# Performance work log

Measured on AMD Instinct MI355X. Metric: run time of the kernel, lower is better.

The kernel has to match this reference:

```python
import jax, jax.numpy as jnp
import numpy as np

EPS = 1e-5
D_MODEL = 64
D_STATE = 16
D_INNER = 128  # expand=2
DT_RANK = 4    # ceil(64/16)


def _inorm(x):
    # InstanceNorm2d (affine=False), NCHW, biased variance, eps=1e-5
    mu = jnp.mean(x, axis=(2, 3), keepdims=True)
    var = jnp.var(x, axis=(2, 3), keepdims=True)
    return (x - mu) * jax.lax.rsqrt(var + EPS)


def _conv2d(x, w, b=None, groups=1):
    y = jax.lax.conv_general_dilated(x, w, (1, 1), 'SAME',
        dimension_numbers=('NCHW', 'OIHW', 'NCHW'), feature_group_count=groups)
    return y if b is None else y + b[None, :, None, None]


def _layernorm(x, w, b):
    mu = jnp.mean(x, axis=-1, keepdims=True)
    var = jnp.var(x, axis=-1, keepdims=True)
    return (x - mu) * jax.lax.rsqrt(var + EPS) * w + b


def _selective_scan(u, delta, A, Bm, Cm, Dp, delta_bias):
    # u, delta: (B,d,L); A: (d,N); Bm,Cm: (B,N,L); Dp: (d,)
    delta = jax.nn.softplus(delta + delta_bias[None, :, None])
    dA = jnp.exp(jnp.einsum('bdl,dn->lbdn', delta, A))        # (L,B,d,N)
    dBu = jnp.einsum('bdl,bnl->lbdn', delta * u, Bm)          # (L,B,d,N)
    Cl = jnp.transpose(Cm, (2, 0, 1))                         # (L,B,N)
    h0 = jnp.zeros((u.shape[0], u.shape[1], A.shape[1]), u.dtype)

    def step(h, inp):
        dA_l, dBu_l, c = inp
        h = dA_l * h + dBu_l
        return h, jnp.einsum('bdn,bn->bd', h, c)

    _, ys = jax.lax.scan(step, h0, (dA, dBu, Cl))             # ys: (L,B,d)
    return jnp.transpose(ys, (1, 2, 0)) + u * Dp[None, :, None]


def _forward(x, dw3_w, dw3_b, dw5_w, dw5_b, dw7_w, dw7_b, fuse_w, fuse_b,
             in_proj_w, conv2d_w, conv2d_b, x_proj_w, dt_proj_w, dt_proj_b,
             A_log, Dp, out_norm_w, out_norm_b, out_proj_w, cf_w, cf_b):
    C = x.shape[1]
    lrelu = lambda t: jax.nn.leaky_relu(t, 0.01)
    # ---- LRGS: multi-scale depthwise convs + fuse + residual (shortcut=Identity) ----
    feats = [lrelu(_inorm(_conv2d(x, w, b, groups=C)))
             for w, b in ((dw3_w, dw3_b), (dw5_w, dw5_b), (dw7_w, dw7_b))]
    xf = _conv2d(jnp.concatenate(feats, axis=1), fuse_w, fuse_b)
    x1 = lrelu(_inorm(xf)) + x
    # ---- MC_Mamba / SS2D ----
    xh = jnp.transpose(x1, (0, 2, 3, 1))           # (B,H,W,C)
    Bn, H, W, _ = xh.shape
    xz = xh @ in_proj_w.T                          # (B,H,W,2*d_inner)
    xm, z = jnp.split(xz, 2, axis=-1)
    xm = jnp.transpose(xm, (0, 3, 1, 2))           # (B,d_inner,H,W)
    xm = jax.nn.silu(_conv2d(xm, conv2d_w, conv2d_b, groups=D_INNER))
    L = H * W
    x_flat = jnp.transpose(xm.reshape(Bn, D_INNER, L), (0, 2, 1))  # (B,L,d)
    xp = x_flat @ x_proj_w.T
    dt, Bm, Cm = jnp.split(xp, [DT_RANK, DT_RANK + D_STATE], axis=-1)
    # NOTE: faithful to source, nn.Linear applies dt_proj_b here AND it is
    # passed again as delta_bias to the scan (bias applied twice).
    dt = jnp.transpose(dt @ dt_proj_w.T + dt_proj_b, (0, 2, 1))    # (B,d,L)
    A = -jnp.exp(A_log)
    y = _selective_scan(jnp.transpose(x_flat, (0, 2, 1)), dt, A,
                        jnp.transpose(Bm, (0, 2, 1)), jnp.transpose(Cm, (0, 2, 1)),
                        Dp, dt_proj_b)
    y = jnp.transpose(y, (0, 2, 1)).reshape(Bn, H, W, D_INNER)
    y = _layernorm(y, out_norm_w, out_norm_b) * jax.nn.silu(z)
    y = y @ out_proj_w.T                           # (B,H,W,d_model)
    y = jnp.transpose(y, (0, 3, 1, 2))
    y = _inorm(_conv2d(y, cf_w, cf_b))
    return x1 + y


def setup_inputs() -> dict:
    key = jax.random.key(0)
    ks = jax.random.split(key, 12)
    B, C, H, W = 8, D_MODEL, 64, 64
    s = 0.05
    return {
        'x': jax.random.normal(ks[0], (B, C, H, W), jnp.float32),
        'dw3_w': jax.random.normal(ks[1], (C, 1, 3, 3), jnp.float32) * s,
        'dw3_b': jnp.zeros((C,), jnp.float32),
        'dw5_w': jax.random.normal(ks[2], (C, 1, 5, 5), jnp.float32) * s,
        'dw5_b': jnp.zeros((C,), jnp.float32),
        'dw7_w': jax.random.normal(ks[3], (C, 1, 7, 7), jnp.float32) * s,
        'dw7_b': jnp.zeros((C,), jnp.float32),
        'fuse_w': jax.random.normal(ks[4], (C, 3 * C, 1, 1), jnp.float32) * s,
        'fuse_b': jnp.zeros((C,), jnp.float32),
        'in_proj_w': jax.random.normal(ks[5], (2 * D_INNER, D_MODEL), jnp.float32) * s,
        'conv2d_w': jax.random.normal(ks[6], (D_INNER, 1, 3, 3), jnp.float32) * s,
        'conv2d_b': jnp.zeros((D_INNER,), jnp.float32),
        'x_proj_w': jax.random.normal(ks[7], (DT_RANK + 2 * D_STATE, D_INNER), jnp.float32) * s,
        'dt_proj_w': jax.random.uniform(ks[8], (D_INNER, DT_RANK), jnp.float32, -0.5, 0.5),
        'dt_proj_b': jnp.exp(jax.random.uniform(ks[9], (D_INNER,), jnp.float32)
                             * (np.log(0.1) - np.log(0.001)) + np.log(0.001)).astype(jnp.float32),
        'A_log': jnp.log(jnp.tile(jnp.arange(1, D_STATE + 1, dtype=jnp.float32), (D_INNER, 1))),
        'Dp': jnp.ones((D_INNER,), jnp.float32),
        'out_norm_w': jnp.ones((D_INNER,), jnp.float32),
        'out_norm_b': jnp.zeros((D_INNER,), jnp.float32),
        'out_proj_w': jax.random.normal(ks[10], (D_MODEL, D_INNER), jnp.float32) * s,
        'cf_w': jax.random.normal(ks[11], (D_MODEL, D_MODEL, 1, 1), jnp.float32) * s,
        'cf_b': jnp.zeros((D_MODEL,), jnp.float32),
    }


def reference(x, dw3_w, dw3_b, dw5_w, dw5_b, dw7_w, dw7_b, fuse_w, fuse_b,
              in_proj_w, conv2d_w, conv2d_b, x_proj_w, dt_proj_w, dt_proj_b,
              A_log, Dp, out_norm_w, out_norm_b, out_proj_w, cf_w, cf_b):
    return _forward(x, dw3_w, dw3_b, dw5_w, dw5_b, dw7_w, dw7_b, fuse_w, fuse_b,
                    in_proj_w, conv2d_w, conv2d_b, x_proj_w, dt_proj_w, dt_proj_b,
                    A_log, Dp, out_norm_w, out_norm_b, out_proj_w, cf_w, cf_b)
```

## Files before the change

kernel.cpp:

```cpp
#include <hip/hip_runtime.h>
#include <math.h>

#define NB 8
#define NC 64
#define NL 4096
#define NDI 128
#define NN 16
#define CHUNK 32
#define NKCH 128

#define OFF_FEATS 0ull
#define OFF_AC    0ull
#define OFF_BC    2097152ull
#define OFF_HINIT 4194304ull
#define OFF_XF    6291456ull
#define OFF_BMAT  6291456ull
#define OFF_CMAT  6815744ull
#define OFF_X1    8388608ull
#define OFF_XMRAW 10485760ull
#define OFF_G     10485760ull
#define OFF_Z     14680064ull
#define OFF_YC    14680064ull
#define OFF_PART  16777216ull
#define OFF_STATS 16809984ull
#define OFF_XMC   18874368ull
#define OFF_DTM   23068672ull
#define OFF_WF    27262976ull
#define OFF_NSTAT (OFF_WF + 55552ull)
#define OFF_WCOMB (OFF_WF + 58624ull)
#define WS_NEED_FLOATS (OFF_WF + 66816ull)

#define WF_DW3    0
#define WF_DW5    576
#define WF_DW7    2176
#define WF_B3     5312
#define WF_B5     5376
#define WF_B7     5440
#define WF_FUSE   5504
#define WF_FUSEB  17792
#define WF_C2W    17856
#define WF_C2B    19008
#define WF_XPW    19136
#define WF_DTW    23744
#define WF_DTB    24256
#define WF_A      24384
#define WF_DP     26432
#define WF_ONW    26560
#define WF_ONB    26688
#define WF_OPW    26816
#define WF_CFW    35008
#define WF_CFB    39104
#define WF_INPJ   39168

struct Cvt { const float* src; float* dst; int n; int op; };
struct CvtArgs { Cvt d[22]; int ncvt; const float* cfw; const float* opw; float* wcomb; };

__global__ __launch_bounds__(256) void k0_cvt(CvtArgs a){
  if ((int)blockIdx.x < a.ncvt){
    Cvt c = a.d[blockIdx.x];
    for (int i = threadIdx.x; i < c.n; i += 256){
      float v = c.src[i];
      c.dst[i] = c.op ? -expf(v) : v;
    }
  } else {
    int idx = (blockIdx.x - a.ncvt)*256 + threadIdx.x;
    int c = idx >> 7, kk = idx & 127;
    float s = 0.f;
    #pragma unroll
    for (int j=0;j<64;j++) s += a.cfw[c*64+j] * a.opw[j*128+kk];
    a.wcomb[idx] = s;
  }
}

__global__ __launch_bounds__(256) void k1_dw(const float* __restrict__ x, const float* __restrict__ wf,
                                             float* __restrict__ feats, float* __restrict__ part){
  const int half = blockIdx.x & 1, c = (blockIdx.x >> 1) & 63, b = blockIdx.x >> 7;
  const int tid = threadIdx.x;
  const int r0 = half*32;
  __shared__ float xs[38*73];
  __shared__ float red[4][6];
  for (int i = tid; i < 38*73; i += 256) xs[i] = 0.f;
  const float* xp = x + ((size_t)b*64 + c)*NL;
  float v[10];
  #pragma unroll
  for (int k=0;k<10;k++){
    int idx = tid + k*256;
    int j = idx >> 6, w = idx & 63;
    int gr = r0 - 3 + j;
    bool ok = (idx < 2432) && (gr >= 0) && (gr < 64);
    v[k] = ok ? xp[gr*64 + w] : 0.f;
  }
  float w3r[9], w5r[25], w7r[49];
  #pragma unroll
  for (int i=0;i<9;i++)  w3r[i] = wf[WF_DW3 + c*9 + i];
  #pragma unroll
  for (int i=0;i<25;i++) w5r[i] = wf[WF_DW5 + c*25 + i];
  #pragma unroll
  for (int i=0;i<49;i++) w7r[i] = wf[WF_DW7 + c*49 + i];
  float b3 = wf[WF_B3+c], b5 = wf[WF_B5+c], b7 = wf[WF_B7+c];
  __syncthreads();
  #pragma unroll
  for (int k=0;k<10;k++){
    int idx = tid + k*256;
    if (idx < 2432){
      int j = idx >> 6, w = idx & 63;
      xs[j*73 + (w+3)] = v[k];
    }
  }
  __syncthreads();
  float s3=0,q3=0,s5=0,q5=0,s7=0,q7=0;
  float* f3 = feats + ((size_t)b*192 + c) * NL + r0*64;
  float* f5 = f3 + (size_t)64*NL;
  float* f7 = f3 + (size_t)128*NL;
  #pragma unroll
  for (int g=0; g<2; g++){
    int p = g*1024 + tid*4;
    int lh = p >> 6, w0 = p & 63;
    float a3[4], a5[4], a7[4];
    #pragma unroll
    for (int i=0;i<4;i++){ a3[i]=b3; a5[i]=b5; a7[i]=b7; }
    #pragma unroll
    for (int dy=0; dy<7; dy++){
      float s[10];
      #pragma unroll
      for (int j=0;j<10;j++) s[j] = xs[(lh+dy)*73 + w0 + j];
      #pragma unroll
      for (int dx=0;dx<7;dx++){
        float wv = w7r[dy*7+dx];
        #pragma unroll
        for (int i=0;i<4;i++) a7[i] += s[dx+i]*wv;
      }
      if (dy>=1 && dy<=5){
        #pragma unroll
        for (int dx=0;dx<5;dx++){
          float wv = w5r[(dy-1)*5+dx];
          #pragma unroll
          for (int i=0;i<4;i++) a5[i] += s[dx+1+i]*wv;
        }
      }
      if (dy>=2 && dy<=4){
        #pragma unroll
        for (int dx=0;dx<3;dx++){
          float wv = w3r[(dy-2)*3+dx];
          #pragma unroll
          for (int i=0;i<4;i++) a3[i] += s[dx+2+i]*wv;
        }
      }
    }
    *(float4*)(f3+p) = make_float4(a3[0],a3[1],a3[2],a3[3]);
    *(float4*)(f5+p) = make_float4(a5[0],a5[1],a5[2],a5[3]);
    *(float4*)(f7+p) = make_float4(a7[0],a7[1],a7[2],a7[3]);
    #pragma unroll
    for (int i=0;i<4;i++){
      s3+=a3[i]; q3+=a3[i]*a3[i];
      s5+=a5[i]; q5+=a5[i]*a5[i];
      s7+=a7[i]; q7+=a7[i]*a7[i];
    }
  }
  int wid = tid>>6, lane = tid&63;
  float v6[6]={s3,q3,s5,q5,s7,q7};
  #pragma unroll
  for (int j=0;j<6;j++){
    float t = v6[j];
    #pragma unroll
    for (int o=32;o>0;o>>=1) t += __shfl_down(t,o);
    if (!lane) red[wid][j]=t;
  }
  __syncthreads();
  if (tid < 3){
    float su = red[0][tid*2]+red[1][tid*2]+red[2][tid*2]+red[3][tid*2];
    float sq = red[0][tid*2+1]+red[1][tid*2+1]+red[2][tid*2+1]+red[3][tid*2+1];
    size_t k = (size_t)(b*192 + tid*64 + c)*4 + half*2;
    part[k]   = su;
    part[k+1] = sq;
  }
}

__global__ __launch_bounds__(256) void k2_fuse(const float* __restrict__ feats, const float* __restrict__ npart,
                                               const float* __restrict__ wf, float* __restrict__ xf){
  int og = blockIdx.x >> 8, rem = blockIdx.x & 255;
  int b = rem >> 5, pt = rem & 31;
  int jslot = threadIdx.x >> 5, pxslot = threadIdx.x & 31;
  __shared__ float wlds[32][192];
  __shared__ float xs[32][128];
  __shared__ float msl[192], rsl[192];
  for (int i = threadIdx.x; i < 192; i += 256){
    const float* pp = npart + (size_t)(b*192+i)*4;
    float su = pp[0]+pp[2], sq = pp[1]+pp[3];
    float m = su*(1.f/NL);
    msl[i] = m;
    rsl[i] = rsqrtf(sq*(1.f/NL) - m*m + 1e-5f);
  }
  {
    const float4* Wg = (const float4*)(wf + WF_FUSE + og*32*192);
    float4* Wl = (float4*)&wlds[0][0];
    for (int i = threadIdx.x; i < 1536; i += 256) Wl[i] = Wg[i];
  }
  float acc[4][4];
  #pragma unroll
  for (int j=0;j<4;j++)
    #pragma unroll
    for (int p=0;p<4;p++) acc[j][p]=0.f;
  const float* fbase = feats + (size_t)b*192*NL + pt*128;
  for (int ch = 0; ch < 6; ch++){
    __syncthreads();
    for (int i = threadIdx.x; i < 1024; i += 256){
      int r = i >> 5, c4 = i & 31;
      int k = ch*32 + r;
      float4 f = *(const float4*)(fbase + (size_t)k*NL + c4*4);
      float m = msl[k], rs = rsl[k];
      float v0=(f.x-m)*rs, v1=(f.y-m)*rs, v2=(f.z-m)*rs, v3=(f.w-m)*rs;
      v0 = v0>0.f?v0:0.01f*v0; v1 = v1>0.f?v1:0.01f*v1;
      v2 = v2>0.f?v2:0.01f*v2; v3 = v3>0.f?v3:0.01f*v3;
      ((float4*)&xs[r][0])[c4] = make_float4(v0,v1,v2,v3);
    }
    __syncthreads();
    #pragma unroll 1
    for (int c = 0; c < 32; c++){
      float a[4];
      #pragma unroll
      for (int p=0;p<4;p++) a[p] = xs[c][pxslot + 32*p];
      #pragma unroll
      for (int jj=0;jj<4;jj++){
        float w = wlds[jslot*4+jj][ch*32+c];
        #pragma unroll
        for (int p=0;p<4;p++) acc[jj][p] += w*a[p];
      }
    }
  }
  #pragma unroll
  for (int jj=0;jj<4;jj++){
    int o = og*32 + jslot*4 + jj;
    float bias = wf[WF_FUSEB + o];
    float* dp = xf + (size_t)b*64*NL + (size_t)o*NL + pt*128;
    #pragma unroll
    for (int p=0;p<4;p++) dp[pxslot + 32*p] = acc[jj][p] + bias;
  }
}

__global__ __launch_bounds__(256) void k3_norm(const float* __restrict__ xf, const float* __restrict__ x,
                                               float* __restrict__ x1){
  const int tid = threadIdx.x;
  const size_t base = (size_t)blockIdx.x * NL;
  float loc[16]; float s=0.f, q=0.f;
  #pragma unroll
  for (int i=0;i<16;i++){ float v = xf[base + tid + i*256]; loc[i]=v; s+=v; q+=v*v; }
  __shared__ float red[4][2];
  int wid = tid>>6, lane = tid&63;
  #pragma unroll
  for (int o=32;o>0;o>>=1){ s += __shfl_down(s,o); q += __shfl_down(q,o); }
  if (!lane){ red[wid][0]=s; red[wid][1]=q; }
  __syncthreads();
  s = red[0][0]+red[1][0]+red[2][0]+red[3][0];
  q = red[0][1]+red[1][1]+red[2][1]+red[3][1];
  float m = s*(1.f/NL), va = q*(1.f/NL)-m*m, rs = rsqrtf(va+1e-5f);
  #pragma unroll
  for (int i=0;i<16;i++){
    int idx = tid + i*256;
    float v = (loc[i]-m)*rs;
    v = v>0.f ? v : 0.01f*v;
    x1[base+idx] = v + x[base+idx];
  }
}

__global__ __launch_bounds__(256) void k4_inproj(const float* __restrict__ x1, const float* __restrict__ wf,
                                                 float* __restrict__ xmraw, float* __restrict__ z){
  int og = blockIdx.x >> 8, rem = blockIdx.x & 255;
  int b = rem >> 5, pt = rem & 31;
  int jslot = threadIdx.x >> 5, pxslot = threadIdx.x & 31;
  __shared__ float wlds[64][64];
  __shared__ float xs[32][128];
  {
    const float4* Wg = (const float4*)(wf + WF_INPJ + og*64*64);
    float4* Wl = (float4*)&wlds[0][0];
    for (int i = threadIdx.x; i < 1024; i += 256) Wl[i] = Wg[i];
  }
  float acc[8][4];
  #pragma unroll
  for (int j=0;j<8;j++)
    #pragma unroll
    for (int p=0;p<4;p++) acc[j][p]=0.f;
  const float* xbase = x1 + (size_t)b*64*NL + pt*128;
  for (int ch = 0; ch < 2; ch++){
    __syncthreads();
    for (int i = threadIdx.x; i < 1024; i += 256){
      int r = i >> 5, c4 = i & 31;
      ((float4*)&xs[r][0])[c4] = *(const float4*)(xbase + (size_t)(ch*32+r)*NL + c4*4);
    }
    __syncthreads();
    #pragma unroll 1
    for (int c = 0; c < 32; c++){
      float a[4];
      #pragma unroll
      for (int p=0;p<4;p++) a[p] = xs[c][pxslot + 32*p];
      #pragma unroll
      for (int jj=0;jj<8;jj++){
        float w = wlds[jslot*8+jj][ch*32+c];
        #pragma unroll
        for (int p=0;p<4;p++) acc[jj][p] += w*a[p];
      }
    }
  }
  float* dstbase = (og < 2 ? xmraw + (size_t)b*128*NL + (size_t)(og*64)*NL
                           : z     + (size_t)b*128*NL + (size_t)((og-2)*64)*NL) + pt*128;
  #pragma unroll
  for (int jj=0;jj<8;jj++){
    float* dp = dstbase + (size_t)(jslot*8+jj)*NL;
    #pragma unroll
    for (int p=0;p<4;p++) dp[pxslot + 32*p] = acc[jj][p];
  }
}

__global__ __launch_bounds__(256) void k5_dw3(const float* __restrict__ xmraw, const float* __restrict__ wf,
                                              float* __restrict__ xmc){
  const int d = blockIdx.x & 127;
  const int tid = threadIdx.x;
  __shared__ float xs[66*69];
  for (int i=tid;i<66*69;i+=256) xs[i]=0.f;
  const float* xp = xmraw + (size_t)blockIdx.x * NL;
  float v[16];
  #pragma unroll
  for (int k=0;k<16;k++) v[k] = xp[tid + k*256];
  float wr[9];
  #pragma unroll
  for (int i=0;i<9;i++) wr[i] = wf[WF_C2W + d*9 + i];
  float bb = wf[WF_C2B + d];
  __syncthreads();
  #pragma unroll
  for (int k=0;k<16;k++){
    int i = tid + k*256;
    int h = i>>6, w = i&63;
    xs[(h+1)*69 + (w+1)] = v[k];
  }
  __syncthreads();
  float* op = xmc + (size_t)blockIdx.x * NL;
  #pragma unroll
  for (int g=0; g<4; g++){
    int p = g*1024 + tid*4;
    int h = p>>6, w0 = p&63;
    float a[4];
    #pragma unroll
    for (int i=0;i<4;i++) a[i]=bb;
    #pragma unroll
    for (int dy=0; dy<3; dy++){
      float s[6];
      #pragma unroll
      for (int j=0;j<6;j++) s[j] = xs[(h+dy)*69 + w0 + j];
      #pragma unroll
      for (int dx=0;dx<3;dx++){
        float wv = wr[dy*3+dx];
        #pragma unroll
        for (int i=0;i<4;i++) a[i] += s[dx+i]*wv;
      }
    }
    float4 o;
    o.x = a[0]/(1.f+__expf(-a[0]));
    o.y = a[1]/(1.f+__expf(-a[1]));
    o.z = a[2]/(1.f+__expf(-a[2]));
    o.w = a[3]/(1.f+__expf(-a[3]));
    *(float4*)(op+p) = o;
  }
}

__global__ __launch_bounds__(256) void k6_xproj(const float* __restrict__ xmc, const float* __restrict__ wf,
                                                float* __restrict__ Bm, float* __restrict__ Cm,
                                                float* __restrict__ dtm){
  int b = blockIdx.x >> 5, pt = blockIdx.x & 31;
  int jslot = threadIdx.x >> 6, pxslot = threadIdx.x & 63;
  __shared__ float wlds[36][128];
  __shared__ float xs[32][128];
  {
    const float4* Wg = (const float4*)(wf + WF_XPW);
    float4* Wl = (float4*)&wlds[0][0];
    for (int i = threadIdx.x; i < 1152; i += 256) Wl[i] = Wg[i];
  }
  float acc[9][2];
  #pragma unroll
  for (int j=0;j<9;j++){ acc[j][0]=0.f; acc[j][1]=0.f; }
  const float* ubase = xmc + (size_t)b*128*NL + pt*128;
  for (int ch = 0; ch < 4; ch++){
    __syncthreads();
    for (int i = threadIdx.x; i < 1024; i += 256){
      int r = i >> 5, c4 = i & 31;
      ((float4*)&xs[r][0])[c4] = *(const float4*)(ubase + (size_t)(ch*32+r)*NL + c4*4);
    }
    __syncthreads();
    #pragma unroll 1
    for (int c = 0; c < 32; c++){
      float a0 = xs[c][pxslot];
      float a1 = xs[c][pxslot + 64];
      #pragma unroll
      for (int j=0;j<9;j++){
        float w = wlds[jslot*9+j][ch*32+c];
        acc[j][0] += w*a0;
        acc[j][1] += w*a1;
      }
    }
  }
  #pragma unroll
  for (int j=0;j<9;j++){
    int o = jslot*9 + j;
    float* dp;
    if (o < 4)       dp = dtm + ((size_t)b*4 + o)*NL;
    else if (o < 20) dp = Bm  + ((size_t)b*16 + (o-4))*NL;
    else             dp = Cm  + ((size_t)b*16 + (o-20))*NL;
    dp[pt*128 + pxslot]      = acc[j][0];
    dp[pt*128 + pxslot + 64] = acc[j][1];
  }
}

__global__ __launch_bounds__(128) void k7_scan1(const float* __restrict__ xmc, const float* __restrict__ Bm,
                                                const float* __restrict__ dtm, const float* __restrict__ wf,
                                                float* __restrict__ Ac, float* __restrict__ Bc){
  int k = blockIdx.x & (NKCH-1), b = blockIdx.x >> 7;
  int d = threadIdx.x;
  int l0 = k*CHUNK;
  __shared__ float xs[128*33];
  __shared__ float Bl2[32*20];
  __shared__ float dtl2[32*4];
  float vx[32], vb[4], vd;
  #pragma unroll
  for (int j=0;j<32;j++){
    int i = d + 128*j;
    int ch = i >> 5, px = i & 31;
    vx[j] = xmc[((size_t)b*128+ch)*NL + l0 + px];
  }
  #pragma unroll
  for (int j=0;j<4;j++){
    int i = d + 128*j;
    int n = i >> 5, li = i & 31;
    vb[j] = Bm[((size_t)b*16+n)*NL + l0 + li];
  }
  { int n = d >> 5, li = d & 31; vd = dtm[((size_t)b*4+n)*NL + l0 + li]; }
  #pragma unroll
  for (int j=0;j<32;j++){
    int i = d + 128*j;
    int ch = i >> 5, px = i & 31;
    xs[ch*33+px] = vx[j];
  }
  #pragma unroll
  for (int j=0;j<4;j++){
    int i = d + 128*j;
    int n = i >> 5, li = i & 31;
    Bl2[li*20+n] = vb[j];
  }
  { int n = d >> 5, li = d & 31; dtl2[li*4+n] = vd; }
  float A[16], P[16], Q[16];
  const float* Af = wf + WF_A + d*16;
  #pragma unroll
  for (int n=0;n<16;n++){ A[n]=Af[n]; P[n]=1.f; Q[n]=0.f; }
  float w0 = wf[WF_DTW+d*4], w1 = wf[WF_DTW+d*4+1], w2 = wf[WF_DTW+d*4+2], w3 = wf[WF_DTW+d*4+3];
  float db2 = 2.f*wf[WF_DTB+d];
  __syncthreads();
  for (int l=0; l<CHUNK; l++){
    float4 dt4 = ((const float4*)dtl2)[l];
    float tt = w0*dt4.x + w1*dt4.y + w2*dt4.z + w3*dt4.w + db2;
    float de = tt > 20.f ? tt : __logf(1.f+__expf(tt));
    float du = de * xs[d*33+l];
    const float4* bp = (const float4*)(Bl2 + l*20);
    float4 b0 = bp[0], b1 = bp[1], b2 = bp[2], b3 = bp[3];
    float bb[16] = {b0.x,b0.y,b0.z,b0.w, b1.x,b1.y,b1.z,b1.w,
                    b2.x,b2.y,b2.z,b2.w, b3.x,b3.y,b3.z,b3.w};
    #pragma unroll
    for (int n=0;n<16;n++){
      float a = __expf(de*A[n]);
      P[n] *= a;
      Q[n] = a*Q[n] + du*bb[n];
    }
  }
  size_t base = (((size_t)k*NB + b)*128 + d)*16;
  #pragma unroll
  for (int i=0;i<4;i++){
    ((float4*)(Ac+base))[i] = make_float4(P[i*4],P[i*4+1],P[i*4+2],P[i*4+3]);
    ((float4*)(Bc+base))[i] = make_float4(Q[i*4],Q[i*4+1],Q[i*4+2],Q[i*4+3]);
  }
}

__global__ __launch_bounds__(256) void k8_mid(const float* __restrict__ Ac, const float* __restrict__ Bc,
                                              float* __restrict__ Hi){
  int idx = blockIdx.x*256 + threadIdx.x;
  float h = 0.f;
  for (int k0=0;k0<NKCH;k0+=16){
    float av[16], bv[16];
    #pragma unroll
    for (int j=0;j<16;j++){
      size_t o = (size_t)(k0+j)*16384 + idx;
      av[j]=Ac[o]; bv[j]=Bc[o];
    }
    #pragma unroll
    for (int j=0;j<16;j++){
      size_t o = (size_t)(k0+j)*16384 + idx;
      Hi[o] = h;
      h = av[j]*h + bv[j];
    }
  }
}

__global__ __launch_bounds__(128) void k9_scan2(const float* __restrict__ xmc, const float* __restrict__ Bm,
                                                const float* __restrict__ Cm, const float* __restrict__ dtm,
                                                const float* __restrict__ z, const float* __restrict__ wf,
                                                const float* __restrict__ Hi, float* __restrict__ G){
  int k = blockIdx.x & (NKCH-1), b = blockIdx.x >> 7;
  int d = threadIdx.x;
  int l0 = k*CHUNK;
  __shared__ float xs[128*33];
  __shared__ float Bl2[32*20], Cl2[32*20];
  __shared__ float dtl2[32*4];
  __shared__ float red[4][32][2];
  __shared__ float mstat[32], rstat[32];
  float vx[32], vb[4], vc[4], vd;
  #pragma unroll
  for (int j=0;j<32;j++){
    int i = d + 128*j;
    int ch = i >> 5, px = i & 31;
    vx[j] = xmc[((size_t)b*128+ch)*NL + l0 + px];
  }
  #pragma unroll
  for (int j=0;j<4;j++){
    int i = d + 128*j;
    int n = i >> 5, li = i & 31;
    vb[j] = Bm[((size_t)b*16+n)*NL + l0 + li];
    vc[j] = Cm[((size_t)b*16+n)*NL + l0 + li];
  }
  { int n = d >> 5, li = d & 31; vd = dtm[((size_t)b*4+n)*NL + l0 + li]; }
  float A[16], h[16];
  const float* Af = wf + WF_A + d*16;
  size_t hb = (((size_t)k*NB + b)*128 + d)*16;
  #pragma unroll
  for (int n=0;n<16;n++){ A[n]=Af[n]; h[n]=Hi[hb+n]; }
  #pragma unroll
  for (int j=0;j<32;j++){
    int i = d + 128*j;
    int ch = i >> 5, px = i & 31;
    xs[ch*33+px] = vx[j];
  }
  #pragma unroll
  for (int j=0;j<4;j++){
    int i = d + 128*j;
    int n = i >> 5, li = i & 31;
    Bl2[li*20+n] = vb[j];
    Cl2[li*20+n] = vc[j];
  }
  { int n = d >> 5, li = d & 31; dtl2[li*4+n] = vd; }
  float Dv = wf[WF_DP + d];
  float w0 = wf[WF_DTW+d*4], w1 = wf[WF_DTW+d*4+1], w2 = wf[WF_DTW+d*4+2], w3 = wf[WF_DTW+d*4+3];
  float db2 = 2.f*wf[WF_DTB+d];
  __syncthreads();
  for (int l=0; l<CHUNK; l++){
    float4 dt4 = ((const float4*)dtl2)[l];
    float tt = w0*dt4.x + w1*dt4.y + w2*dt4.z + w3*dt4.w + db2;
    float de = tt > 20.f ? tt : __logf(1.f+__expf(tt));
    float uu = xs[d*33+l];
    float du = de * uu;
    float yv = uu * Dv;
    const float4* bp = (const float4*)(Bl2 + l*20);
    const float4* cp = (const float4*)(Cl2 + l*20);
    float4 b0 = bp[0], b1 = bp[1], b2 = bp[2], b3 = bp[3];
    float4 c0 = cp[0], c1 = cp[1], c2 = cp[2], c3 = cp[3];
    float bb[16] = {b0.x,b0.y,b0.z,b0.w, b1.x,b1.y,b1.z,b1.w,
                    b2.x,b2.y,b2.z,b2.w, b3.x,b3.y,b3.z,b3.w};
    float cc[16] = {c0.x,c0.y,c0.z,c0.w, c1.x,c1.y,c1.z,c1.w,
                    c2.x,c2.y,c2.z,c2.w, c3.x,c3.y,c3.z,c3.w};
    #pragma unroll
    for (int n=0;n<16;n++){
      float a = __expf(de*A[n]);
      h[n] = a*h[n] + du*bb[n];
      yv  += h[n]*cc[n];
    }
    xs[d*33+l] = yv;
  }
  __syncthreads();
  {
    int px = d & 31, q = d >> 5;
    float s=0.f, qq=0.f;
    #pragma unroll
    for (int j=0;j<32;j++){ float v = xs[(q*32+j)*33+px]; s+=v; qq+=v*v; }
    red[q][px][0]=s; red[q][px][1]=qq;
  }
  __syncthreads();
  if (d < 32){
    float ss = red[0][d][0]+red[1][d][0]+red[2][d][0]+red[3][d][0];
    float sq = red[0][d][1]+red[1][d][1]+red[2][d][1]+red[3][d][1];
    float m = ss*(1.f/128.f);
    mstat[d] = m;
    rstat[d] = rsqrtf(sq*(1.f/128.f) - m*m + 1e-5f);
  }
  __syncthreads();
  float ow = wf[WF_ONW+d], ob = wf[WF_ONB+d];
  const float* zp = z + ((size_t)b*128+d)*NL + l0;
  float* gp = G + ((size_t)b*128+d)*NL + l0;
  #pragma unroll
  for (int l4=0; l4<CHUNK/4; l4++){
    float4 zv4 = ((const float4*)zp)[l4];
    float zv[4] = {zv4.x, zv4.y, zv4.z, zv4.w};
    float out[4];
    #pragma unroll
    for (int j=0;j<4;j++){
      int l = l4*4+j;
      float t = (xs[d*33+l]-mstat[l])*rstat[l]*ow + ob;
      out[j] = t * (zv[j]/(1.f+__expf(-zv[j])));
    }
    ((float4*)gp)[l4] = make_float4(out[0],out[1],out[2],out[3]);
  }
}

__global__ __launch_bounds__(256) void k11A_proj(const float* __restrict__ G, const float* __restrict__ wf,
                                                 const float* __restrict__ wcomb,
                                                 float* __restrict__ yc, float* __restrict__ part){
  int og = blockIdx.x >> 8, rem = blockIdx.x & 255;
  int b = rem >> 5, pt = rem & 31;
  int jslot = threadIdx.x >> 5, pxslot = threadIdx.x & 31;
  __shared__ float wlds[32][128];
  __shared__ float xs[32][128];
  {
    const float4* Wg = (const float4*)(wcomb + og*32*128);
    float4* Wl = (float4*)&wlds[0][0];
    for (int i = threadIdx.x; i < 1024; i += 256) Wl[i] = Wg[i];
  }
  float acc[4][4];
  #pragma unroll
  for (int j=0;j<4;j++)
    #pragma unroll
    for (int p=0;p<4;p++) acc[j][p]=0.f;
  const float* gbase = G + (size_t)b*128*NL + pt*128;
  for (int ch = 0; ch < 4; ch++){
    __syncthreads();
    for (int i = threadIdx.x; i < 1024; i += 256){
      int r = i >> 5, c4 = i & 31;
      ((float4*)&xs[r][0])[c4] = *(const float4*)(gbase + (size_t)(ch*32+r)*NL + c4*4);
    }
    __syncthreads();
    #pragma unroll 1
    for (int c = 0; c < 32; c++){
      float a[4];
      #pragma unroll
      for (int p=0;p<4;p++) a[p] = xs[c][pxslot + 32*p];
      #pragma unroll
      for (int jj=0;jj<4;jj++){
        float w = wlds[jslot*4+jj][ch*32+c];
        #pragma unroll
        for (int p=0;p<4;p++) acc[jj][p] += w*a[p];
      }
    }
  }
  #pragma unroll
  for (int jj=0;jj<4;jj++){
    int cc = og*32 + jslot*4 + jj;
    float bias = wf[WF_CFB + cc];
    float* dp = yc + (size_t)b*64*NL + (size_t)cc*NL + pt*128;
    float sv = 0.f, qv = 0.f;
    #pragma unroll
    for (int p=0;p<4;p++){
      float t = acc[jj][p] + bias;
      dp[pxslot + 32*p] = t;
      sv += t; qv += t*t;
    }
    #pragma unroll
    for (int o=16;o>0;o>>=1){ sv += __shfl_xor(sv,o); qv += __shfl_xor(qv,o); }
    if (pxslot == 0){
      size_t pidx = (((size_t)b*64 + cc)*32 + pt)*2;
      part[pidx] = sv; part[pidx+1] = qv;
    }
  }
}

__global__ __launch_bounds__(256) void k11b_stats(const float* __restrict__ part, float* __restrict__ stats){
  int i = blockIdx.x*256 + threadIdx.x;
  if (i >= 512) return;
  float s=0.f, q=0.f;
  #pragma unroll
  for (int t2=0;t2<32;t2++){ s += part[((size_t)i*32+t2)*2]; q += part[((size_t)i*32+t2)*2+1]; }
  float m = s*(1.f/NL), va = q*(1.f/NL) - m*m;
  stats[i*2] = m; stats[i*2+1] = rsqrtf(va+1e-5f);
}

__global__ __launch_bounds__(256) void k11c_final(const float* __restrict__ yc, const float* __restrict__ stats,
                                                  const float* __restrict__ x1, float* __restrict__ out){
  int bc = blockIdx.x;
  float m = stats[bc*2], rs = stats[bc*2+1];
  size_t base = (size_t)bc*NL;
  for (int i=threadIdx.x;i<NL;i+=256){
    float v = (yc[base+i]-m)*rs;
    out[base+i] = x1[base+i] + v;
  }
}

extern "C" void kernel_launch(void* const* d_in, const int* in_sizes, int n_in,
                              void* d_out, int out_size, void* d_ws, size_t ws_size,
                              hipStream_t stream) {
  if (ws_size < WS_NEED_FLOATS * sizeof(float)) return;
  const float* x     = (const float*)d_in[0];
  const float* dw3w  = (const float*)d_in[1];
  const float* dw3b  = (const float*)d_in[2];
  const float* dw5w  = (const float*)d_in[3];
  const float* dw5b  = (const float*)d_in[4];
  const float* dw7w  = (const float*)d_in[5];
  const float* dw7b  = (const float*)d_in[6];
  const float* fusew = (const float*)d_in[7];
  const float* fuseb = (const float*)d_in[8];
  const float* inpjw = (const float*)d_in[9];
  const float* c2w   = (const float*)d_in[10];
  const float* c2b   = (const float*)d_in[11];
  const float* xpw   = (const float*)d_in[12];
  const float* dtw   = (const float*)d_in[13];
  const float* dtb   = (const float*)d_in[14];
  const float* alog  = (const float*)d_in[15];
  const float* dpv   = (const float*)d_in[16];
  const float* onw   = (const float*)d_in[17];
  const float* onb   = (const float*)d_in[18];
  const float* opw   = (const float*)d_in[19];
  const float* cfw   = (const float*)d_in[20];
  const float* cfb   = (const float*)d_in[21];

  float* ws    = (float*)d_ws;
  float* wf    = ws + OFF_WF;
  float* wcomb = ws + OFF_WCOMB;
  float* feats = ws + OFF_FEATS;
  float* xf    = ws + OFF_XF;
  float* x1    = ws + OFF_X1;
  float* xmraw = ws + OFF_XMRAW;
  float* z     = ws + OFF_Z;
  float* xmc   = ws + OFF_XMC;
  float* Bmw   = ws + OFF_BMAT;
  float* Cmw   = ws + OFF_CMAT;
  float* dtm   = ws + OFF_DTM;
  float* Acb   = ws + OFF_AC;
  float* Bcb   = ws + OFF_BC;
  float* Hi    = ws + OFF_HINIT;
  float* G     = ws + OFF_G;
  float* yc    = ws + OFF_YC;
  float* part  = ws + OFF_PART;
  float* stats = ws + OFF_STATS;

  CvtArgs ca; int ns = 0;
  auto add = [&](const float* s, int off, int n, int op){
    ca.d[ns].src = s; ca.d[ns].dst = wf + off; ca.d[ns].n = n; ca.d[ns].op = op; ns++;
  };
  add(dw3w, WF_DW3, 576, 0);   add(dw5w, WF_DW5, 1600, 0);  add(dw7w, WF_DW7, 3136, 0);
  add(dw3b, WF_B3, 64, 0);     add(dw5b, WF_B5, 64, 0);     add(dw7b, WF_B7, 64, 0);
  add(fusew, WF_FUSE, 12288, 0); add(fuseb, WF_FUSEB, 64, 0);
  add(c2w, WF_C2W, 1152, 0);   add(c2b, WF_C2B, 128, 0);
  add(xpw, WF_XPW, 4608, 0);   add(dtw, WF_DTW, 512, 0);    add(dtb, WF_DTB, 128, 0);
  add(alog, WF_A, 2048, 1);
  add(dpv, WF_DP, 128, 0);
  add(onw, WF_ONW, 128, 0);    add(onb, WF_ONB, 128, 0);
  add(opw, WF_OPW, 8192, 0);
  add(cfw, WF_CFW, 4096, 0);   add(cfb, WF_CFB, 64, 0);
  add(inpjw, WF_INPJ, 16384, 0);
  ca.ncvt = ns; ca.cfw = cfw; ca.opw = opw; ca.wcomb = wcomb;

  k0_cvt<<<ns + 32, 256, 0, stream>>>(ca);
  k1_dw<<<1024, 256, 0, stream>>>(x, wf, feats, part);
  k2_fuse<<<512, 256, 0, stream>>>(feats, part, wf, xf);
  k3_norm<<<512, 256, 0, stream>>>(xf, x, x1);
  k4_inproj<<<1024, 256, 0, stream>>>(x1, wf, xmraw, z);
  k5_dw3<<<1024, 256, 0, stream>>>(xmraw, wf, xmc);
  k6_xproj<<<256, 256, 0, stream>>>(xmc, wf, Bmw, Cmw, dtm);
  k7_scan1<<<1024, 128, 0, stream>>>(xmc, Bmw, dtm, wf, Acb, Bcb);
  k8_mid<<<64, 256, 0, stream>>>(Acb, Bcb, Hi);
  k9_scan2<<<1024, 128, 0, stream>>>(xmc, Bmw, Cmw, dtm, z, wf, Hi, G);
  k11A_proj<<<512, 256, 0, stream>>>(G, wf, wcomb, yc, part);
  k11b_stats<<<2, 256, 0, stream>>>(part, stats);
  k11c_final<<<512, 256, 0, stream>>>(yc, stats, x1, (float*)d_out);
}
```

Measured before the change: 213.6 us.

## Parallelize chunk-carry scan hierarchically and transpose GEMM weights in LDS for vector loads

The serial mid-scan over 128 chunks, which ran in only 64 blocks, is split into three kernels: per-segment products and offsets across 512 blocks, a short 8-step carry scan, and a parallel emit of the initial states. This gives the latency-bound serial loop more parallelism, at the cost of an extra read of Ac/Bc and two more launches. Separately, the pointwise GEMM kernels (fuse, in_proj, x_proj, final proj) store their weights transposed and padded in LDS. Each thread can then fetch its output weights with float4 loads instead of scalar strided reads, while the staging loop becomes scalar and uses a transposed write pattern.

```diff
diff --git a/kernel.cpp b/kernel.cpp
--- a/kernel.cpp
+++ b/kernel.cpp
@@ -25,6 +25,9 @@
 #define OFF_STATS 16809984ull
 #define OFF_XMC   18874368ull
 #define OFF_DTM   23068672ull
+#define OFF_SEGP  23199744ull
+#define OFF_SEGQ  23330816ull
+#define OFF_SEGH  23461888ull
 #define OFF_WF    27262976ull
 #define OFF_NSTAT (OFF_WF + 55552ull)
 #define OFF_WCOMB (OFF_WF + 58624ull)
@@ -181,7 +184,7 @@
   int og = blockIdx.x >> 8, rem = blockIdx.x & 255;
   int b = rem >> 5, pt = rem & 31;
   int jslot = threadIdx.x >> 5, pxslot = threadIdx.x & 31;
-  __shared__ float wlds[32][192];
+  __shared__ float wlds2[192][44];
   __shared__ float xs[32][128];
   __shared__ float msl[192], rsl[192];
   for (int i = threadIdx.x; i < 192; i += 256){
@@ -192,9 +195,11 @@
     rsl[i] = rsqrtf(sq*(1.f/NL) - m*m + 1e-5f);
   }
   {
-    const float4* Wg = (const float4*)(wf + WF_FUSE + og*32*192);
-    float4* Wl = (float4*)&wlds[0][0];
-    for (int i = threadIdx.x; i < 1536; i += 256) Wl[i] = Wg[i];
+    const float* Wg = wf + WF_FUSE + og*32*192;
+    for (int i = threadIdx.x; i < 6144; i += 256){
+      int o = i / 192, k = i % 192;
+      wlds2[k][o] = Wg[i];
+    }
   }
   float acc[4][4];
   #pragma unroll
@@ -220,12 +225,12 @@
       float a[4];
       #pragma unroll
       for (int p=0;p<4;p++) a[p] = xs[c][pxslot + 32*p];
-      #pragma unroll
-      for (int jj=0;jj<4;jj++){
-        float w = wlds[jslot*4+jj][ch*32+c];
+      float4 w4 = *(const float4*)&wlds2[ch*32+c][jslot*4];
+      float wv[4] = {w4.x, w4.y, w4.z, w4.w};
+      #pragma unroll
+      for (int jj=0;jj<4;jj++)
         #pragma unroll
-        for (int p=0;p<4;p++) acc[jj][p] += w*a[p];
-      }
+        for (int p=0;p<4;p++) acc[jj][p] += wv[jj]*a[p];
     }
   }
   #pragma unroll
@@ -268,12 +273,14 @@
   int og = blockIdx.x >> 8, rem = blockIdx.x & 255;
   int b = rem >> 5, pt = rem & 31;
   int jslot = threadIdx.x >> 5, pxslot = threadIdx.x & 31;
-  __shared__ float wlds[64][64];
+  __shared__ float wlds2[64][76];
   __shared__ float xs[32][128];
   {
-    const float4* Wg = (const float4*)(wf + WF_INPJ + og*64*64);
-    float4* Wl = (float4*)&wlds[0][0];
-    for (int i = threadIdx.x; i < 1024; i += 256) Wl[i] = Wg[i];
+    const float* Wg = wf + WF_INPJ + og*64*64;
+    for (int i = threadIdx.x; i < 4096; i += 256){
+      int o = i >> 6, k = i & 63;
+      wlds2[k][o] = Wg[i];
+    }
   }
   float acc[8][4];
   #pragma unroll
@@ -293,12 +300,13 @@
       float a[4];
       #pragma unroll
       for (int p=0;p<4;p++) a[p] = xs[c][pxslot + 32*p];
-      #pragma unroll
-      for (int jj=0;jj<8;jj++){
-        float w = wlds[jslot*8+jj][ch*32+c];
+      const float4* wp = (const float4*)&wlds2[ch*32+c][jslot*8];
+      float4 w0 = wp[0], w1 = wp[1];
+      float wv[8] = {w0.x,w0.y,w0.z,w0.w, w1.x,w1.y,w1.z,w1.w};
+      #pragma unroll
+      for (int jj=0;jj<8;jj++)
         #pragma unroll
-        for (int p=0;p<4;p++) acc[jj][p] += w*a[p];
-      }
+        for (int p=0;p<4;p++) acc[jj][p] += wv[jj]*a[p];
     }
   }
   float* dstbase = (og < 2 ? xmraw + (size_t)b*128*NL + (size_t)(og*64)*NL
@@ -367,12 +375,14 @@
                                                 float* __restrict__ dtm){
   int b = blockIdx.x >> 5, pt = blockIdx.x & 31;
   int jslot = threadIdx.x >> 6, pxslot = threadIdx.x & 63;
-  __shared__ float wlds[36][128];
+  __shared__ float wlds2[128][52];
   __shared__ float xs[32][128];
   {
-    const float4* Wg = (const float4*)(wf + WF_XPW);
-    float4* Wl = (float4*)&wlds[0][0];
-    for (int i = threadIdx.x; i < 1152; i += 256) Wl[i] = Wg[i];
+    const float* Wg = wf + WF_XPW;
+    for (int i = threadIdx.x; i < 4608; i += 256){
+      int o = i >> 7, k = i & 127;
+      wlds2[k][(o/9)*12 + (o%9)] = Wg[i];
+    }
   }
   float acc[9][2];
   #pragma unroll
@@ -389,11 +399,15 @@
     for (int c = 0; c < 32; c++){
       float a0 = xs[c][pxslot];
       float a1 = xs[c][pxslot + 64];
+      const float* wr = &wlds2[ch*32+c][jslot*12];
+      float4 wa = *(const float4*)wr;
+      float4 wb = *(const float4*)(wr+4);
+      float w8 = wr[8];
+      float wv[9] = {wa.x,wa.y,wa.z,wa.w, wb.x,wb.y,wb.z,wb.w, w8};
       #pragma unroll
       for (int j=0;j<9;j++){
-        float w = wlds[jslot*9+j][ch*32+c];
-        acc[j][0] += w*a0;
-        acc[j][1] += w*a1;
+        acc[j][0] += wv[j]*a0;
+        acc[j][1] += wv[j]*a1;
       }
     }
   }
@@ -476,23 +490,49 @@
   }
 }
 
-__global__ __launch_bounds__(256) void k8_mid(const float* __restrict__ Ac, const float* __restrict__ Bc,
-                                              float* __restrict__ Hi){
+__global__ __launch_bounds__(256) void k8a_seg(const float* __restrict__ Ac, const float* __restrict__ Bc,
+                                               float* __restrict__ segP, float* __restrict__ segQ){
+  int idx = (blockIdx.x & 63)*256 + threadIdx.x;
+  int seg = blockIdx.x >> 6;
+  float av[16], bv[16];
+  #pragma unroll
+  for (int j=0;j<16;j++){
+    size_t o = (size_t)(seg*16+j)*16384 + idx;
+    av[j]=Ac[o]; bv[j]=Bc[o];
+  }
+  float P = 1.f, Q = 0.f;
+  #pragma unroll
+  for (int j=0;j<16;j++){ Q = av[j]*Q + bv[j]; P *= av[j]; }
+  segP[seg*16384+idx]=P; segQ[seg*16384+idx]=Q;
+}
+
+__global__ __launch_bounds__(256) void k8b_mid(const float* __restrict__ segP, const float* __restrict__ segQ,
+                                               float* __restrict__ segH){
   int idx = blockIdx.x*256 + threadIdx.x;
+  float p[8], q[8];
+  #pragma unroll
+  for (int s=0;s<8;s++){ p[s]=segP[s*16384+idx]; q[s]=segQ[s*16384+idx]; }
   float h = 0.f;
-  for (int k0=0;k0<NKCH;k0+=16){
-    float av[16], bv[16];
-    #pragma unroll
-    for (int j=0;j<16;j++){
-      size_t o = (size_t)(k0+j)*16384 + idx;
-      av[j]=Ac[o]; bv[j]=Bc[o];
-    }
-    #pragma unroll
-    for (int j=0;j<16;j++){
-      size_t o = (size_t)(k0+j)*16384 + idx;
-      Hi[o] = h;
-      h = av[j]*h + bv[j];
-    }
+  #pragma unroll
+  for (int s=0;s<8;s++){ segH[s*16384+idx]=h; h = p[s]*h + q[s]; }
+}
+
+__global__ __launch_bounds__(256) void k8c_emit(const float* __restrict__ Ac, const float* __restrict__ Bc,
+                                                const float* __restrict__ segH, float* __restrict__ Hi){
+  int idx = (blockIdx.x & 63)*256 + threadIdx.x;
+  int seg = blockIdx.x >> 6;
+  float av[16], bv[16];
+  #pragma unroll
+  for (int j=0;j<16;j++){
+    size_t o = (size_t)(seg*16+j)*16384 + idx;
+    av[j]=Ac[o]; bv[j]=Bc[o];
+  }
+  float h = segH[seg*16384+idx];
+  #pragma unroll
+  for (int j=0;j<16;j++){
+    size_t o = (size_t)(seg*16+j)*16384 + idx;
+    Hi[o] = h;
+    h = av[j]*h + bv[j];
   }
 }
 
@@ -610,12 +650,14 @@
   int og = blockIdx.x >> 8, rem = blockIdx.x & 255;
   int b = rem >> 5, pt = rem & 31;
   int jslot = threadIdx.x >> 5, pxslot = threadIdx.x & 31;
-  __shared__ float wlds[32][128];
+  __shared__ float wlds2[128][44];
   __shared__ float xs[32][128];
   {
-    const float4* Wg = (const float4*)(wcomb + og*32*128);
-    float4* Wl = (float4*)&wlds[0][0];
-    for (int i = threadIdx.x; i < 1024; i += 256) Wl[i] = Wg[i];
+    const float* Wg = wcomb + og*32*128;
+    for (int i = threadIdx.x; i < 4096; i += 256){
+      int o = i >> 7, k = i & 127;
+      wlds2[k][o] = Wg[i];
+    }
   }
   float acc[4][4];
   #pragma unroll
@@ -635,12 +677,12 @@
       float a[4];
       #pragma unroll
       for (int p=0;p<4;p++) a[p] = xs[c][pxslot + 32*p];
-      #pragma unroll
-      for (int jj=0;jj<4;jj++){
-        float w = wlds[jslot*4+jj][ch*32+c];
+      float4 w4 = *(const float4*)&wlds2[ch*32+c][jslot*4];
+      float wv[4] = {w4.x, w4.y, w4.z, w4.w};
+      #pragma unroll
+      for (int jj=0;jj<4;jj++)
         #pragma unroll
-        for (int p=0;p<4;p++) acc[jj][p] += w*a[p];
-      }
+        for (int p=0;p<4;p++) acc[jj][p] += wv[jj]*a[p];
     }
   }
   #pragma unroll
@@ -727,6 +769,9 @@
   float* Acb   = ws + OFF_AC;
   float* Bcb   = ws + OFF_BC;
   float* Hi    = ws + OFF_HINIT;
+  float* segP  = ws + OFF_SEGP;
+  float* segQ  = ws + OFF_SEGQ;
+  float* segH  = ws + OFF_SEGH;
   float* G     = ws + OFF_G;
   float* yc    = ws + OFF_YC;
   float* part  = ws + OFF_PART;
@@ -757,7 +802,9 @@
   k5_dw3<<<1024, 256, 0, stream>>>(xmraw, wf, xmc);
   k6_xproj<<<256, 256, 0, stream>>>(xmc, wf, Bmw, Cmw, dtm);
   k7_scan1<<<1024, 128, 0, stream>>>(xmc, Bmw, dtm, wf, Acb, Bcb);
-  k8_mid<<<64, 256, 0, stream>>>(Acb, Bcb, Hi);
+  k8a_seg<<<512, 256, 0, stream>>>(Acb, Bcb, segP, segQ);
+  k8b_mid<<<64, 256, 0, stream>>>(segP, segQ, segH);
+  k8c_emit<<<512, 256, 0, stream>>>(Acb, Bcb, segH, Hi);
   k9_scan2<<<1024, 128, 0, stream>>>(xmc, Bmw, Cmw, dtm, z, wf, Hi, G);
   k11A_proj<<<512, 256, 0, stream>>>(G, wf, wcomb, yc, part);
   k11b_stats<<<2, 256, 0, stream>>>(part, stats);
```

Result: no change. 212.7 us (-0.4%).
